# Kernel optimization log

Hardware: AMD Instinct MI355X
Metric: run time of the kernel (lower is better)

## Reference

```python
import jax, jax.numpy as jnp
import numpy as np

B, N, C = 64, 197, 768
H = 12
L, KAPPA = 4, 16


def setup_inputs() -> dict:
    key = jax.random.key(0)
    ks = jax.random.split(key, 7)
    src = jax.random.normal(ks[0], (B, N, C), jnp.float32)
    vtm_memory = jax.random.normal(ks[1], (L, B, KAPPA, C), jnp.float32)
    Wq = jax.random.normal(ks[2], (C, C), jnp.float32) * 0.02
    Wk = jax.random.normal(ks[3], (C, C), jnp.float32) * 0.02
    Wv = jax.random.normal(ks[4], (C, C), jnp.float32) * 0.02
    Wp = jax.random.normal(ks[5], (C, C), jnp.float32) * 0.02
    bp = jnp.zeros((C,), jnp.float32)
    return {"src": src, "vtm_memory": vtm_memory, "Wq": Wq, "Wk": Wk, "Wv": Wv, "Wp": Wp, "bp": bp}


def reference(src, vtm_memory, Wq, Wk, Wv, Wp, bp):
    Bb, Nn, Cc = src.shape
    hd = Cc // H
    scale = hd ** -0.5
    Ll, _, Tt, _ = vtm_memory.shape
    # stack per-layer memories -> [B, L*kappa, C], concat with src as KV
    vtm_tokens = vtm_memory.transpose(1, 0, 2, 3).reshape(Bb, Ll * Tt, Cc)
    kv = jnp.concatenate([src, vtm_tokens], axis=1)  # [B, N+L*kappa, C]
    Nkv = kv.shape[1]
    # VTM_ATTN cross-attention (bias-free qkv, biased proj; dropout = identity)
    q = (src @ Wq.T).reshape(Bb, Nn, H, hd).transpose(0, 2, 1, 3)    # [B,H,N,hd]
    k = (kv @ Wk.T).reshape(Bb, Nkv, H, hd).transpose(0, 2, 1, 3)    # [B,H,Nkv,hd]
    v = (kv @ Wv.T).reshape(Bb, Nkv, H, hd).transpose(0, 2, 1, 3)
    attn = jax.nn.softmax(jnp.einsum('bhqd,bhkd->bhqk', q, k) * scale, axis=-1)
    attn_out = attn[:, :, :, :Nn]  # self-part slice, detached in original
    x = jnp.einsum('bhqk,bhkd->bhqd', attn, v).transpose(0, 2, 1, 3).reshape(Bb, Nn, Cc)
    x = x @ Wp.T + bp
    # register_memory: CLS-row saliency over non-CLS keys, topk gather from src
    saliency = attn_out.mean(axis=1)[:, 0, 1:]          # [B, N-1]
    _, top_idx = jax.lax.top_k(saliency, KAPPA)          # [B, kappa]
    salient_tokens = jnp.take_along_axis(src, top_idx[:, :, None], axis=1)  # [B, kappa, C]
    return (x, attn_out, salient_tokens)
```

## Files before the change

kernel.cpp:

```cpp
#include <hip/hip_runtime.h>
#include <cstdint>

typedef _Float16 half8 __attribute__((ext_vector_type(8)));
typedef float f32x4 __attribute__((ext_vector_type(4)));
typedef unsigned short u16;

#define B_ 64
#define NQ 197
#define C_ 768
#define H_ 12
#define NKV 261
#define RKV 16768
#define RQ  12672

#define X_OFF    0
#define ATTN_OFF 9682944
#define SAL_OFF  39488256

#define WS_WQKV  0u
#define WS_WP    3538944u
#define WS_KV    4718592u
#define WS_QKV   30474240u
#define WS_O     107741184u
#define WS_Q0    (WS_KV + 0u)
#define WS_P     (WS_KV + 196608u)
#define WS_R     (WS_KV + 1048576u)

__device__ __forceinline__ u16 f2h(float f) {
  return __builtin_bit_cast(u16, (_Float16)f);
}

__global__ void wconv(const float* __restrict__ Wq, const float* __restrict__ Wk,
                      const float* __restrict__ Wv, const float* __restrict__ Wp,
                      u16* __restrict__ Wqkv, u16* __restrict__ Wph) {
  for (int i = blockIdx.x * blockDim.x + threadIdx.x; i < 4 * 147456;
       i += gridDim.x * blockDim.x) {
    int g = i / 147456;
    int idx = (i - g * 147456) * 4;
    const float* s = (g == 0) ? Wq : (g == 1) ? Wk : (g == 2) ? Wv : Wp;
    float4 v = *(const float4*)(s + idx);
    union { u16 u[4]; uint64_t q; } o;
    o.u[0] = f2h(v.x); o.u[1] = f2h(v.y); o.u[2] = f2h(v.z); o.u[3] = f2h(v.w);
    u16* d = (g < 3) ? (Wqkv + (size_t)g * 589824 + idx) : (Wph + idx);
    *(uint64_t*)d = o.q;
  }
}

__global__ void build_kv(const float* __restrict__ src, const float* __restrict__ vtm,
                         u16* __restrict__ kvh) {
  const int total = RKV * 192;
  for (int i = blockIdx.x * blockDim.x + threadIdx.x; i < total;
       i += gridDim.x * blockDim.x) {
    int row = i / 192;
    int c = (i - row * 192) * 4;
    union { u16 u[4]; uint64_t q; } o;
    if (row < B_ * NKV) {
      int b = row / NKV, t = row - b * NKV;
      const float* p;
      if (t < NQ) p = src + ((size_t)b * NQ + t) * 768 + c;
      else {
        int tt = t - NQ;
        p = vtm + ((size_t)((tt >> 4) * 64 + b) * 16 + (tt & 15)) * 768 + c;
      }
      float4 v = *(const float4*)p;
      o.u[0] = f2h(v.x); o.u[1] = f2h(v.y); o.u[2] = f2h(v.z); o.u[3] = f2h(v.w);
    } else {
      o.q = 0;
    }
    *(uint64_t*)(kvh + (size_t)row * 768 + c) = o.q;
  }
}

template <int EPI>
__launch_bounds__(256, 2)
__global__ void gemm_bt(const u16* __restrict__ A, const u16* __restrict__ Bw,
                        void* __restrict__ Cp, const float* __restrict__ bias,
                        int mtiles, int kdim, int lda, int ldb, int ldc, int mlimit) {
  __shared__ u16 sA[128 * 32];
  __shared__ u16 sB[128 * 32];
  const int tid = threadIdx.x;
  const int w = tid >> 6, lane = tid & 63;
  const int bid = blockIdx.x;
  const int mt = bid % mtiles, nt = bid / mtiles;
  const int srow = tid >> 2, scol = (tid & 3) << 3;
  const u16* gA = A + (size_t)(mt * 128 + srow) * lda + scol;
  const u16* gB = Bw + (size_t)(nt * 128 + srow) * ldb + scol;
  const int wr = w >> 1, wc = w & 1;
  const int fr = lane & 15, fc = (lane >> 4) << 3;

  const f32x4 vz = {0.f, 0.f, 0.f, 0.f};
  f32x4 acc[4][4];
#pragma unroll
  for (int i = 0; i < 4; ++i)
#pragma unroll
    for (int j = 0; j < 4; ++j) acc[i][j] = vz;

  for (int k0 = 0; k0 < kdim; k0 += 32) {
    uint4 va0 = *(const uint4*)(gA + k0);
    uint4 va1 = *(const uint4*)(gA + (size_t)64 * lda + k0);
    uint4 vb0 = *(const uint4*)(gB + k0);
    uint4 vb1 = *(const uint4*)(gB + (size_t)64 * ldb + k0);
    __syncthreads();
    *(uint4*)((char*)sA + tid * 16) = va0;
    *(uint4*)((char*)sA + 4096 + tid * 16) = va1;
    *(uint4*)((char*)sB + tid * 16) = vb0;
    *(uint4*)((char*)sB + 4096 + tid * 16) = vb1;
    __syncthreads();
    half8 af[4], bf[4];
#pragma unroll
    for (int i = 0; i < 4; ++i) {
      af[i] = *(const half8*)&sA[(wr * 64 + i * 16 + fr) * 32 + fc];
      bf[i] = *(const half8*)&sB[(wc * 64 + i * 16 + fr) * 32 + fc];
    }
#pragma unroll
    for (int mi = 0; mi < 4; ++mi)
#pragma unroll
      for (int ni = 0; ni < 4; ++ni)
        acc[mi][ni] = __builtin_amdgcn_mfma_f32_16x16x32_f16(af[mi], bf[ni], acc[mi][ni], 0, 0, 0);
  }

  const int rbase = (lane >> 4) << 2;
#pragma unroll
  for (int mi = 0; mi < 4; ++mi) {
#pragma unroll
    for (int ni = 0; ni < 4; ++ni) {
      const int n = nt * 128 + wc * 64 + ni * 16 + fr;
#pragma unroll
      for (int r = 0; r < 4; ++r) {
        const int m = mt * 128 + wr * 64 + mi * 16 + rbase + r;
        if (EPI == 0) {
          ((u16*)Cp)[(size_t)m * ldc + n] = f2h(acc[mi][ni][r]);
        } else {
          if (m < mlimit) ((float*)Cp)[(size_t)m * ldc + n] = acc[mi][ni][r] + bias[n];
        }
      }
    }
  }
}

#define ATT_LDS_TOT 79872

__launch_bounds__(256, 2)
__global__ void attn_kernel(const u16* __restrict__ qkv, float* __restrict__ out,
                            u16* __restrict__ Oh) {
  extern __shared__ char smem[];
  const int tid = threadIdx.x, w = tid >> 6, lane = tid & 63;
  const int bid = blockIdx.x;
  const int b = bid / 12, h = bid - b * 12;
  const size_t rowbase = (size_t)b * NKV;

  for (int i = tid; i < 272 * 8; i += 256) {
    const int row = i >> 3, c8 = (i & 7) << 3;
    uint4 v = *(const uint4*)(qkv + (rowbase + row) * 2304 + 768 + h * 64 + c8);
    *(uint4*)(smem + row * 128 + ((c8 * 2) ^ ((row & 7) << 4))) = v;
  }
  for (int i = tid; i < 288 * 8; i += 256) {
    const int row = i >> 3, c8 = (i & 7) << 3;
    union { u16 u[8]; uint4 v; } t;
    t.v = *(const uint4*)(qkv + (rowbase + row) * 2304 + 1536 + h * 64 + c8);
#pragma unroll
    for (int j = 0; j < 8; ++j) {
      const int d = c8 + j;
      const int sw = ((row < 256) ? (d & 7) : (d & 3)) << 4;
      *(u16*)(smem + 34816 + d * 576 + ((row * 2) ^ sw)) = t.u[j];
    }
  }
  __syncthreads();

  const int fr = lane & 15, g = lane >> 4;
  char* PcBase = smem + 71680 + (w << 11);
  const f32x4 vz = {0.f, 0.f, 0.f, 0.f};

  for (int qt = w; qt < 13; qt += 4) {
    const u16* qp = qkv + (rowbase + qt * 16 + fr) * 2304 + h * 64 + g * 8;
    half8 aq0 = *(const half8*)qp;
    half8 aq1 = *(const half8*)(qp + 32);

    f32x4 sc[17];
#pragma unroll
    for (int jt = 0; jt < 17; ++jt) {
      const int krow = jt * 16 + fr;
      const int swz = (krow & 7) << 4;
      half8 bk0 = *(const half8*)(smem + krow * 128 + ((g * 16) ^ swz));
      half8 bk1 = *(const half8*)(smem + krow * 128 + ((64 + g * 16) ^ swz));
      f32x4 a = vz;
      a = __builtin_amdgcn_mfma_f32_16x16x32_f16(aq0, bk0, a, 0, 0, 0);
      a = __builtin_amdgcn_mfma_f32_16x16x32_f16(aq1, bk1, a, 0, 0, 0);
      sc[jt] = a;
    }
#pragma unroll
    for (int jt = 0; jt < 17; ++jt) {
      const bool valid = (jt * 16 + fr) < NKV;
#pragma unroll
      for (int ri = 0; ri < 4; ++ri)
        sc[jt][ri] = valid ? sc[jt][ri] * 0.125f : -3.0e38f;
    }
#pragma unroll
    for (int ri = 0; ri < 4; ++ri) {
      float m = sc[0][ri];
#pragma unroll
      for (int jt = 1; jt < 17; ++jt) m = fmaxf(m, sc[jt][ri]);
#pragma unroll
      for (int off = 1; off <= 8; off <<= 1) m = fmaxf(m, __shfl_xor(m, off, 64));
      float s = 0.f;
#pragma unroll
      for (int jt = 0; jt < 17; ++jt) {
        float e = __expf(sc[jt][ri] - m);
        sc[jt][ri] = e;
        s += e;
      }
#pragma unroll
      for (int off = 1; off <= 8; off <<= 1) s += __shfl_xor(s, off, 64);
      const float inv = 1.f / s;
#pragma unroll
      for (int jt = 0; jt < 17; ++jt) sc[jt][ri] *= inv;
    }
    const int q0r = qt * 16 + g * 4;
    {
      float* ob = out + ATTN_OFF + (size_t)bid * NQ * NQ;
#pragma unroll
      for (int jt = 0; jt < 13; ++jt) {
        const int col = jt * 16 + fr;
        if (col < NQ) {
#pragma unroll
          for (int ri = 0; ri < 4; ++ri) {
            const int qr = q0r + ri;
            if (qr < NQ) ob[(size_t)qr * NQ + col] = sc[jt][ri];
          }
        }
      }
    }
    f32x4 oa[4] = {vz, vz, vz, vz};
#pragma unroll
    for (int kt = 0; kt < 9; ++kt) {
      char* pcb = PcBase + (kt & 1) * 1024;
#pragma unroll
      for (int hf = 0; hf < 2; ++hf) {
        const int jt = kt * 2 + hf;
#pragma unroll
        for (int ri = 0; ri < 4; ++ri) {
          const int prow = g * 4 + ri, pcol = hf * 16 + fr;
          const float v = (jt < 17) ? sc[jt][ri] : 0.f;
          *(u16*)(pcb + prow * 64 + ((pcol * 2) ^ ((prow & 3) << 4))) = f2h(v);
        }
      }
      asm volatile("s_waitcnt lgkmcnt(0)" ::: "memory");
      __builtin_amdgcn_sched_barrier(0);
      half8 pa = *(const half8*)(pcb + fr * 64 + ((g * 16) ^ ((fr & 3) << 4)));
#pragma unroll
      for (int dt = 0; dt < 4; ++dt) {
        const int vrow = dt * 16 + fr;
        const int sw = ((kt < 8) ? (vrow & 7) : (vrow & 3)) << 4;
        half8 bv = *(const half8*)(smem + 34816 + vrow * 576 + ((kt * 64 + g * 16) ^ sw));
        oa[dt] = __builtin_amdgcn_mfma_f32_16x16x32_f16(pa, bv, oa[dt], 0, 0, 0);
      }
    }
#pragma unroll
    for (int dt = 0; dt < 4; ++dt)
#pragma unroll
      for (int ri = 0; ri < 4; ++ri) {
        const int qr = q0r + ri;
        if (qr < NQ)
          Oh[((size_t)b * NQ + qr) * 768 + h * 64 + dt * 16 + fr] = f2h(oa[dt][ri]);
      }
  }
}

__global__ void sal_q0(const float* __restrict__ src, const float* __restrict__ Wq,
                       float* __restrict__ q0ws) {
  const int bid = blockIdx.x;
  const int b = bid / 192, cb = (bid - (bid / 192) * 192) * 4;
  const int w = threadIdx.x >> 6, lane = threadIdx.x & 63;
  const int c = cb + w;
  const float* srow = src + (size_t)b * NQ * 768;
  const float* wrow = Wq + (size_t)c * 768;
  float acc = 0.f;
#pragma unroll
  for (int j = 0; j < 12; ++j)
    acc = fmaf(srow[lane + 64 * j], wrow[lane + 64 * j], acc);
#pragma unroll
  for (int off = 32; off >= 1; off >>= 1) acc += __shfl_xor(acc, off, 64);
  if (lane == 0) q0ws[(size_t)b * 768 + c] = acc;
}

__global__ void sal_r(const float* __restrict__ q0ws, const float* __restrict__ Wk,
                      float* __restrict__ rws) {
  const int bid = blockIdx.x;
  const int b = bid / 36, rem = bid - (bid / 36) * 36;
  const int h = rem / 3, cc = (rem - (rem / 3) * 3) * 256;
  const int c = cc + threadIdx.x;
  __shared__ float sq[64];
  if (threadIdx.x < 64) sq[threadIdx.x] = q0ws[(size_t)b * 768 + h * 64 + threadIdx.x];
  __syncthreads();
  float acc = 0.f;
#pragma unroll
  for (int dh = 0; dh < 64; ++dh)
    acc = fmaf(sq[dh], Wk[(size_t)(h * 64 + dh) * 768 + c], acc);
  rws[((size_t)b * 12 + h) * 768 + c] = acc;
}

__global__ void sal_p(const float* __restrict__ src, const float* __restrict__ vtm,
                      const float* __restrict__ rws, float* __restrict__ pws) {
  const int bid = blockIdx.x;
  const int b = bid / NKV, kk = bid - (bid / NKV) * NKV;
  const int w = threadIdx.x >> 6, lane = threadIdx.x & 63;
  const float* kvrow;
  if (kk < NQ) kvrow = src + ((size_t)b * NQ + kk) * 768;
  else {
    int tt = kk - NQ;
    kvrow = vtm + ((size_t)((tt >> 4) * 64 + b) * 16 + (tt & 15)) * 768;
  }
  float v[12];
#pragma unroll
  for (int j = 0; j < 12; ++j) v[j] = kvrow[lane + 64 * j];
  for (int hh = w; hh < 12; hh += 4) {
    const float* rrow = rws + ((size_t)b * 12 + hh) * 768;
    float acc = 0.f;
#pragma unroll
    for (int j = 0; j < 12; ++j) acc = fmaf(v[j], rrow[lane + 64 * j], acc);
#pragma unroll
    for (int off = 32; off >= 1; off >>= 1) acc += __shfl_xor(acc, off, 64);
    if (lane == 0) pws[((size_t)b * 12 + hh) * NKV + kk] = acc * 0.125f;
  }
}

__global__ void sal_top(const float* __restrict__ src, const float* __restrict__ pws,
                        float* __restrict__ out) {
  const int b = blockIdx.x, tid = threadIdx.x, w = tid >> 6, lane = tid & 63;
  __shared__ float s_p[12][272];
  __shared__ float s_sal[196];
  __shared__ int s_top[16];
  for (int i = tid; i < 12 * NKV; i += 256)
    s_p[i / NKV][i - (i / NKV) * NKV] = pws[(size_t)b * 12 * NKV + i];
  __syncthreads();
  for (int hh = w; hh < 12; hh += 4) {
    float m = -3.0e38f;
    for (int kk = lane; kk < NKV; kk += 64) m = fmaxf(m, s_p[hh][kk]);
#pragma unroll
    for (int off = 32; off >= 1; off >>= 1) m = fmaxf(m, __shfl_xor(m, off, 64));
    float s = 0.f;
    for (int kk = lane; kk < NKV; kk += 64) s += expf(s_p[hh][kk] - m);
#pragma unroll
    for (int off = 32; off >= 1; off >>= 1) s += __shfl_xor(s, off, 64);
    for (int kk = lane; kk < NKV; kk += 64) s_p[hh][kk] = expf(s_p[hh][kk] - m) / s;
  }
  __syncthreads();
  if (tid < 196) {
    float a = 0.f;
#pragma unroll
    for (int hh = 0; hh < 12; ++hh) a += s_p[hh][tid + 1];
    s_sal[tid] = a * (1.0f / 12.0f);
  }
  __syncthreads();
  if (w == 0) {
    float v[4];
    int idx[4];
    bool taken[4];
#pragma unroll
    for (int j = 0; j < 4; ++j) {
      int id = lane + 64 * j;
      idx[j] = id;
      taken[j] = false;
      v[j] = (id < 196) ? s_sal[id] : -3.0e38f;
    }
    for (int round = 0; round < 16; ++round) {
      float best = -3.0e38f;
      int bi = 1 << 30;
#pragma unroll
      for (int j = 0; j < 4; ++j)
        if (!taken[j] && v[j] > best) { best = v[j]; bi = idx[j]; }
#pragma unroll
      for (int off = 1; off <= 32; off <<= 1) {
        float ov = __shfl_xor(best, off, 64);
        int oi = __shfl_xor(bi, off, 64);
        if (ov > best || (ov == best && oi < bi)) { best = ov; bi = oi; }
      }
#pragma unroll
      for (int j = 0; j < 4; ++j)
        if (idx[j] == bi) taken[j] = true;
      if (lane == 0) s_top[round] = bi;
    }
  }
  __syncthreads();
  for (int i = 0; i < 16; ++i) {
    int id = s_top[i];
    for (int c = tid; c < 768; c += 256)
      out[SAL_OFF + ((size_t)b * 16 + i) * 768 + c] = src[((size_t)b * NQ + id) * 768 + c];
  }
}

extern "C" void kernel_launch(void* const* d_in, const int* in_sizes, int n_in,
                              void* d_out, int out_size, void* d_ws, size_t ws_size,
                              hipStream_t stream) {
  const float* src = (const float*)d_in[0];
  const float* vtm = (const float*)d_in[1];
  const float* Wq = (const float*)d_in[2];
  const float* Wk = (const float*)d_in[3];
  const float* Wv = (const float*)d_in[4];
  const float* Wp = (const float*)d_in[5];
  const float* bp = (const float*)d_in[6];
  float* out = (float*)d_out;
  char* ws = (char*)d_ws;

  u16* Wqkv = (u16*)(ws + WS_WQKV);
  u16* Wph = (u16*)(ws + WS_WP);
  u16* kvh = (u16*)(ws + WS_KV);
  u16* QKV = (u16*)(ws + WS_QKV);
  u16* Oh = (u16*)(ws + WS_O);
  float* q0ws = (float*)(ws + WS_Q0);
  float* pws = (float*)(ws + WS_P);
  float* rws = (float*)(ws + WS_R);

  wconv<<<1152, 256, 0, stream>>>(Wq, Wk, Wv, Wp, Wqkv, Wph);
  build_kv<<<2048, 256, 0, stream>>>(src, vtm, kvh);
  gemm_bt<0><<<131 * 18, 256, 0, stream>>>(kvh, Wqkv, QKV, nullptr, 131, 768, 768, 768, 2304, 0);
  hipFuncSetAttribute((const void*)attn_kernel, hipFuncAttributeMaxDynamicSharedMemorySize,
                      ATT_LDS_TOT);
  attn_kernel<<<B_ * H_, 256, ATT_LDS_TOT, stream>>>(QKV, out, Oh);
  gemm_bt<1><<<99 * 6, 256, 0, stream>>>(Oh, Wph, out, bp, 99, 768, 768, 768, 768, 12608);
  sal_q0<<<64 * 192, 256, 0, stream>>>(src, Wq, q0ws);
  sal_r<<<64 * 12 * 3, 256, 0, stream>>>(q0ws, Wk, rws);
  sal_p<<<64 * NKV, 256, 0, stream>>>(src, vtm, rws, pws);
  sal_top<<<64, 256, 0, stream>>>(src, pws, out);
}
```

Before: 335.7 us.

## Use direct global-to-LDS loads with swizzled K=64 tiles and XCD-aware block remap

Reworks the GEMM main loop to load tiles straight from global memory into LDS with global_load_lds, instead of staging them through registers. The K step doubles to 64 and an XOR swizzle is applied to the LDS layout to avoid bank conflicts on the fragment reads. Block IDs are remapped so neighbouring tiles land on the same XCD for better L2 reuse, and launch bounds are raised to 4 waves per SIMD. The trade-off is twice the LDS per block, which may cap occupancy, while there is still no double buffering to overlap loads with MFMA work.

```diff
diff --git a/kernel.cpp b/kernel.cpp
--- a/kernel.cpp
+++ b/kernel.cpp
@@ -4,6 +4,11 @@
 typedef _Float16 half8 __attribute__((ext_vector_type(8)));
 typedef float f32x4 __attribute__((ext_vector_type(4)));
 typedef unsigned short u16;
+
+typedef __attribute__((address_space(3))) char lds_char;
+typedef const __attribute__((address_space(1))) char glb_char;
+#define GLOAD16(gp, lp) \
+  __builtin_amdgcn_global_load_lds((glb_char*)(gp), (lds_char*)(lp), 16, 0, 0)
 
 #define B_ 64
 #define NQ 197
@@ -72,21 +77,36 @@
 }
 
 template <int EPI>
-__launch_bounds__(256, 2)
+__launch_bounds__(256, 4)
 __global__ void gemm_bt(const u16* __restrict__ A, const u16* __restrict__ Bw,
                         void* __restrict__ Cp, const float* __restrict__ bias,
                         int mtiles, int kdim, int lda, int ldb, int ldc, int mlimit) {
-  __shared__ u16 sA[128 * 32];
-  __shared__ u16 sB[128 * 32];
+  __shared__ u16 sA[128 * 64];
+  __shared__ u16 sB[128 * 64];
   const int tid = threadIdx.x;
   const int w = tid >> 6, lane = tid & 63;
-  const int bid = blockIdx.x;
+  int bid = blockIdx.x;
+  {
+    const int nwg = gridDim.x;
+    const int q = nwg >> 3, rr = nwg & 7;
+    const int xcd = bid & 7, loc = bid >> 3;
+    bid = (xcd < rr ? xcd * (q + 1) : rr * (q + 1) + (xcd - rr) * q) + loc;
+  }
   const int mt = bid % mtiles, nt = bid / mtiles;
-  const int srow = tid >> 2, scol = (tid & 3) << 3;
-  const u16* gA = A + (size_t)(mt * 128 + srow) * lda + scol;
-  const u16* gB = Bw + (size_t)(nt * 128 + srow) * ldb + scol;
   const int wr = w >> 1, wc = w & 1;
-  const int fr = lane & 15, fc = (lane >> 4) << 3;
+  const int fr = lane & 15, g = lane >> 4;
+  const int frs = fr & 7;
+
+  const u16* gAp[4];
+  const u16* gBp[4];
+#pragma unroll
+  for (int j = 0; j < 4; ++j) {
+    const int lin = j * 256 + tid;
+    const int r = lin >> 3;
+    const int c = (lin & 7) ^ (r & 7);
+    gAp[j] = A + (size_t)(mt * 128 + r) * lda + c * 8;
+    gBp[j] = Bw + (size_t)(nt * 128 + r) * ldb + c * 8;
+  }
 
   const f32x4 vz = {0.f, 0.f, 0.f, 0.f};
   f32x4 acc[4][4];
@@ -95,28 +115,31 @@
 #pragma unroll
     for (int j = 0; j < 4; ++j) acc[i][j] = vz;
 
-  for (int k0 = 0; k0 < kdim; k0 += 32) {
-    uint4 va0 = *(const uint4*)(gA + k0);
-    uint4 va1 = *(const uint4*)(gA + (size_t)64 * lda + k0);
-    uint4 vb0 = *(const uint4*)(gB + k0);
-    uint4 vb1 = *(const uint4*)(gB + (size_t)64 * ldb + k0);
+  for (int k0 = 0; k0 < kdim; k0 += 64) {
     __syncthreads();
-    *(uint4*)((char*)sA + tid * 16) = va0;
-    *(uint4*)((char*)sA + 4096 + tid * 16) = va1;
-    *(uint4*)((char*)sB + tid * 16) = vb0;
-    *(uint4*)((char*)sB + 4096 + tid * 16) = vb1;
+#pragma unroll
+    for (int j = 0; j < 4; ++j)
+      GLOAD16(gAp[j] + k0, ((char*)sA) + (j * 256 + tid) * 16);
+#pragma unroll
+    for (int j = 0; j < 4; ++j)
+      GLOAD16(gBp[j] + k0, ((char*)sB) + (j * 256 + tid) * 16);
     __syncthreads();
-    half8 af[4], bf[4];
-#pragma unroll
-    for (int i = 0; i < 4; ++i) {
-      af[i] = *(const half8*)&sA[(wr * 64 + i * 16 + fr) * 32 + fc];
-      bf[i] = *(const half8*)&sB[(wc * 64 + i * 16 + fr) * 32 + fc];
-    }
-#pragma unroll
-    for (int mi = 0; mi < 4; ++mi)
-#pragma unroll
-      for (int ni = 0; ni < 4; ++ni)
-        acc[mi][ni] = __builtin_amdgcn_mfma_f32_16x16x32_f16(af[mi], bf[ni], acc[mi][ni], 0, 0, 0);
+#pragma unroll
+    for (int kk = 0; kk < 2; ++kk) {
+      half8 af[4], bf[4];
+      const int sw = ((kk * 4 + g) ^ frs) * 8;
+#pragma unroll
+      for (int i = 0; i < 4; ++i) {
+        af[i] = *(const half8*)&sA[(wr * 64 + i * 16 + fr) * 64 + sw];
+        bf[i] = *(const half8*)&sB[(wc * 64 + i * 16 + fr) * 64 + sw];
+      }
+#pragma unroll
+      for (int mi = 0; mi < 4; ++mi)
+#pragma unroll
+        for (int ni = 0; ni < 4; ++ni)
+          acc[mi][ni] =
+              __builtin_amdgcn_mfma_f32_16x16x32_f16(af[mi], bf[ni], acc[mi][ni], 0, 0, 0);
+    }
   }
 
   const int rbase = (lane >> 4) << 2;
```

Result: faster. 314.5 us (-6.3%).
